# Kernel tuning notes

Hardware: AMD Instinct MI355X
Metric: run time of the kernel (lower is better)

Reference implementation:

```python
import jax, jax.numpy as jnp
import numpy as np

N_NODES = 40000
N_EDGES = 640000
IN_DIM, H_DIM, OUT_DIM = 128, 128, 64


def setup_inputs() -> dict:
    key = jax.random.key(0)
    ks = jax.random.split(key, 16)
    x = jax.random.normal(ks[0], (N_NODES, IN_DIM), dtype=jnp.float32)
    edge_index = jax.random.randint(ks[1], (2, N_EDGES), 0, N_NODES, dtype=jnp.int64)
    dims = [(IN_DIM, H_DIM), (H_DIM, H_DIM), (H_DIM, OUT_DIM)]
    inp = {"x": x, "edge_index": edge_index}
    for l, (di, do) in enumerate(dims):
        s = 1.0 / np.sqrt(di)
        inp[f"Wr{l}"] = jax.random.uniform(ks[2 + 3 * l], (di, do), jnp.float32, -s, s)  # lin_rel weight
        inp[f"br{l}"] = jax.random.uniform(ks[3 + 3 * l], (do,), jnp.float32, -s, s)     # lin_rel bias
        inp[f"Ws{l}"] = jax.random.uniform(ks[4 + 3 * l], (di, do), jnp.float32, -s, s)  # lin_root weight (no bias)
    return inp


def _graph_conv(x, src, dst, Wr, br, Ws):
    # PyG GraphConv (aggr='add'): out = lin_rel(sum_{j in N(i)} x_j) + lin_root(x_i)
    agg = jax.ops.segment_sum(x[src], dst, num_segments=N_NODES)  # [N, d_in]
    return agg @ Wr + br + x @ Ws


def reference(x, edge_index, Wr0, br0, Ws0, Wr1, br1, Ws1, Wr2, br2, Ws2):
    src, dst = edge_index[0], edge_index[1]
    h = x
    for Wr, br, Ws in ((Wr0, br0, Ws0), (Wr1, br1, Ws1), (Wr2, br2, Ws2)):
        h = _graph_conv(h, src, dst, Wr, br, Ws)
        h = jax.nn.relu(h)
        # dropout p=0 / eval mode -> identity
    return jax.nn.log_softmax(h, axis=1)
```

## Files before the change

kernel.cpp:

```cpp
#include <hip/hip_runtime.h>
#include <hip/hip_bf16.h>


#define N_NODES 40000
#define N_EDGES 640000
#define PAD_NODES 40064
#define DEG_CAP   40960
#define ROW_CAP   64

typedef float v4f __attribute__((ext_vector_type(4)));
typedef float v2f __attribute__((ext_vector_type(2)));
typedef short short8 __attribute__((ext_vector_type(8)));

__device__ inline unsigned short f2b(float f) {
    unsigned u = __float_as_uint(f);
    return (unsigned short)((u + 0x7fffu + ((u >> 16) & 1u)) >> 16);
}

__device__ inline unsigned b2f8(unsigned short us) {
    unsigned s  = ((unsigned)us >> 8) & 0x80u;
    unsigned mag = us & 0x7fffu;
    unsigned e8 = mag >> 7, m7 = mag & 0x7fu;
    unsigned out;
    if (e8 < 121u) out = 0u;
    else if (e8 > 135u) out = 0x7eu;
    else {
        unsigned e4 = e8 - 120u;
        unsigned r  = (m7 + 7u + ((m7 >> 4) & 1u)) >> 4;
        if (r == 8u) { r = 0u; e4++; }
        out = (e4 > 15u || (e4 == 15u && r > 6u)) ? 0x7eu : ((e4 << 3) | r);
    }
    return s | out;
}

__device__ inline unsigned pack4_fp8(float f0, float f1, float f2, float f3) {
#if __has_builtin(__builtin_amdgcn_cvt_pk_fp8_f32)
    int w = __builtin_amdgcn_cvt_pk_fp8_f32(f0, f1, 0, false);
    w = __builtin_amdgcn_cvt_pk_fp8_f32(f2, f3, w, true);
    return (unsigned)w;
#else
    return b2f8(f2b(f0)) | (b2f8(f2b(f1)) << 8) |
           (b2f8(f2b(f2)) << 16) | (b2f8(f2b(f3)) << 24);
#endif
}

#if __has_builtin(__builtin_amdgcn_cvt_f32_fp8)
#define F8TOF(w, sel) __builtin_amdgcn_cvt_f32_fp8((int)(w), (sel))
#else
__device__ inline float f8tof_(unsigned b) {
    unsigned e = (b >> 3) & 15u;
    unsigned bits = ((b & 0x80u) << 24) |
                    (e ? (((e + 120u) << 23) | ((b & 7u) << 20)) : 0u);
    return __uint_as_float(bits);
}
#define F8TOF(w, sel) f8tof_(((unsigned)(w) >> ((sel) * 8)) & 0xffu)
#endif

__global__ __launch_bounds__(256) void prep_kernel(const float* __restrict__ Wr0, const float* __restrict__ Ws0,
                                                   const float* __restrict__ Wr1, const float* __restrict__ Ws1,
                                                   const float* __restrict__ Wr2, const float* __restrict__ Ws2,
                                                   const float* __restrict__ x,
                                                   unsigned short* __restrict__ Wt0,
                                                   unsigned short* __restrict__ Wt1,
                                                   unsigned short* __restrict__ Wt2,
                                                   unsigned short* __restrict__ Xb,
                                                   int* __restrict__ deg) {
    int tid = blockIdx.x * 256 + threadIdx.x;
    if (tid < DEG_CAP / 4) {
        ((int4*)deg)[tid] = make_int4(0, 0, 0, 0);
        return;
    }
    int t = tid - DEG_CAP / 4;
    if (t < 32768) {
        int n = t >> 7, k = t & 127;
        const float* W = (n < 128) ? Wr0 : Ws0;
        Wt0[t] = f2b(W[k * 128 + (n & 127)]);
    } else if (t < 65536) {
        int u = t - 32768;
        int n = u >> 7, k = u & 127;
        const float* W = (n < 128) ? Wr1 : Ws1;
        Wt1[u] = f2b(W[k * 128 + (n & 127)]);
    } else if (t < 81920) {
        int u = t - 65536;
        int n = u >> 7, k = u & 127;
        const float* W = (n < 64) ? Wr2 : Ws2;
        Wt2[u] = f2b(W[k * 64 + (n & 63)]);
    } else {
        int u = t - 81920;
        if (u < (N_NODES * 128) / 8) {
            float4 a = ((const float4*)x)[u * 2];
            float4 b = ((const float4*)x)[u * 2 + 1];
            uint4 o;
            o.x = (unsigned)f2b(a.x) | ((unsigned)f2b(a.y) << 16);
            o.y = (unsigned)f2b(a.z) | ((unsigned)f2b(a.w) << 16);
            o.z = (unsigned)f2b(b.x) | ((unsigned)f2b(b.y) << 16);
            o.w = (unsigned)f2b(b.z) | ((unsigned)f2b(b.w) << 16);
            ((uint4*)Xb)[u] = o;
        }
    }
}

__global__ __launch_bounds__(256) void place_kernel(const int* __restrict__ src,
                                                    const int* __restrict__ dst,
                                                    int* __restrict__ deg,
                                                    int* __restrict__ esrc) {
    int e = blockIdx.x * 256 + threadIdx.x;
    if (e < N_EDGES) {
        int d = dst[e];
        int r = atomicAdd(&deg[d], 1);
        if (r < ROW_CAP) esrc[(size_t)d * ROW_CAP + r] = src[e];
    }
}

template <int DO>
__global__ __launch_bounds__(256, 6) void mm_kernel(const unsigned short* __restrict__ Ab,
                                                    const unsigned short* __restrict__ Wt,
                                                    void* __restrict__ Tout,
                                                    unsigned short* __restrict__ S) {
    __shared__ unsigned short Smem[64 * 64 + 128 * 64];
    unsigned short* As = Smem;
    unsigned short* Bs = Smem + 64 * 64;

    const int tid = threadIdx.x;
    const int m0  = blockIdx.x * 64;
    const int n0  = blockIdx.y * 128;

    const int wave = tid >> 6;
    const int lane = tid & 63;
    const int wc   = wave * 32;
    const int qm   = lane & 15;
    const int k8   = (lane >> 4) * 8;

    v4f acc[4][2];
#pragma unroll
    for (int i = 0; i < 4; i++)
#pragma unroll
        for (int j = 0; j < 2; j++) acc[i][j] = (v4f)(0.0f);

#pragma unroll
    for (int half = 0; half < 2; half++) {
#pragma unroll
        for (int i = 0; i < 2; i++) {
            int idx = i * 256 + tid;
            int row = idx >> 3, c8 = idx & 7;
            ((uint4*)As)[idx] =
                *(const uint4*)(Ab + (size_t)(m0 + row) * 128 + half * 64 + c8 * 8);
        }
#pragma unroll
        for (int i = 0; i < 4; i++) {
            int idx = i * 256 + tid;
            int row = idx >> 3, c8 = idx & 7;
            ((uint4*)Bs)[idx] =
                *(const uint4*)(Wt + (size_t)(n0 + row) * 128 + half * 64 + c8 * 8);
        }
        __syncthreads();

#pragma unroll
        for (int ks = 0; ks < 2; ks++) {
            short8 af[4], bf[2];
#pragma unroll
            for (int i = 0; i < 4; i++)
                af[i] = *(const short8*)(const void*)(As + (i * 16 + qm) * 64 + ks * 32 + k8);
#pragma unroll
            for (int j = 0; j < 2; j++)
                bf[j] = *(const short8*)(const void*)(Bs + (wc + j * 16 + qm) * 64 + ks * 32 + k8);
#pragma unroll
            for (int mi = 0; mi < 4; mi++)
#pragma unroll
                for (int ni = 0; ni < 2; ni++)
                    acc[mi][ni] = __builtin_amdgcn_mfma_f32_16x16x32_bf16(af[mi], bf[ni], acc[mi][ni], 0, 0, 0);
        }
        __syncthreads();
    }

#pragma unroll
    for (int mi = 0; mi < 4; mi++) {
        const int rowBase = mi * 16 + ((lane >> 4) << 2);
#pragma unroll
        for (int r = 0; r < 4; r++) {
            const int row = rowBase + r;
            const int sw  = ((row >> 2) & 3) << 4;
#pragma unroll
            for (int ni = 0; ni < 2; ni++) {
                const int c = wc + ni * 16 + qm;
                Smem[row * 128 + (c ^ sw)] = f2b(acc[mi][ni][r]);
            }
        }
    }
    __syncthreads();

    if (DO == 128 && n0 == 0) {
        unsigned char* T8 = (unsigned char*)Tout;
#pragma unroll
        for (int i = 0; i < 2; i++) {
            const int chunk = i * 256 + tid;
            const int row   = chunk >> 3;
            const int c0    = (chunk & 7) * 16;
            const int sw    = ((row >> 2) & 3) << 4;
            const int node  = m0 + row;
            if (node <= N_NODES) {
                uint4 v = make_uint4(0, 0, 0, 0);
                if (node < N_NODES) {
                    const unsigned short* p = Smem + row * 128 + (c0 ^ sw);
                    uint4 ha = *(const uint4*)p;
                    uint4 hb = *(const uint4*)(p + 8);
#define LOF(d) __uint_as_float((d) << 16)
#define HIF(d) __uint_as_float((d) & 0xffff0000u)
                    v.x = pack4_fp8(LOF(ha.x), HIF(ha.x), LOF(ha.y), HIF(ha.y));
                    v.y = pack4_fp8(LOF(ha.z), HIF(ha.z), LOF(ha.w), HIF(ha.w));
                    v.z = pack4_fp8(LOF(hb.x), HIF(hb.x), LOF(hb.y), HIF(hb.y));
                    v.w = pack4_fp8(LOF(hb.z), HIF(hb.z), LOF(hb.w), HIF(hb.w));
#undef LOF
#undef HIF
                }
                *(uint4*)(T8 + (size_t)node * 128 + c0) = v;
            }
        }
    } else {
        unsigned short* T = (unsigned short*)Tout;
#pragma unroll
        for (int i = 0; i < 4; i++) {
            const int chunk = i * 256 + tid;
            const int row   = chunk >> 4;
            const int c0    = (chunk & 15) * 8;
            const int sw    = ((row >> 2) & 3) << 4;
            const int node  = m0 + row;
            if (node <= N_NODES) {
                uint4 v = make_uint4(0, 0, 0, 0);
                if (node < N_NODES)
                    v = *(const uint4*)(Smem + row * 128 + (c0 ^ sw));
                if (DO == 128) {
                    *(uint4*)(S + (size_t)node * 128 + c0) = v;
                } else {
                    if (c0 < 64) *(uint4*)(T + (size_t)node * 64 + c0) = v;
                    else         *(uint4*)(S + (size_t)node * 64 + (c0 - 64)) = v;
                }
            }
        }
    }
}

__device__ inline void addp(v2f* a, uint4 q) {
    v2f t0 = { __uint_as_float(q.x << 16), __uint_as_float(q.x & 0xffff0000u) };
    v2f t1 = { __uint_as_float(q.y << 16), __uint_as_float(q.y & 0xffff0000u) };
    v2f t2 = { __uint_as_float(q.z << 16), __uint_as_float(q.z & 0xffff0000u) };
    v2f t3 = { __uint_as_float(q.w << 16), __uint_as_float(q.w & 0xffff0000u) };
    a[0] += t0; a[1] += t1; a[2] += t2; a[3] += t3;
}
__device__ inline void addp8w(v2f* a, unsigned w) {
    v2f t0 = { F8TOF(w, 0), F8TOF(w, 1) };
    v2f t1 = { F8TOF(w, 2), F8TOF(w, 3) };
    a[0] += t0; a[1] += t1;
}
__device__ inline void addp16(v2f* a, uint4 q) {
    addp8w(a + 0, q.x); addp8w(a + 2, q.y);
    addp8w(a + 4, q.z); addp8w(a + 6, q.w);
}

template <int DO, bool LAST, bool FP8T>
__global__ __launch_bounds__(256) void aggregate_kernel(const void* __restrict__ Tin,
                                                        const unsigned short* __restrict__ S,
                                                        const float* __restrict__ br,
                                                        const int* __restrict__ deg,
                                                        const int* __restrict__ esrc,
                                                        unsigned short* __restrict__ Hout,
                                                        float* __restrict__ Fout) {
    constexpr int DPL = FP8T ? 16 : 8;
    const int lane16 = threadIdx.x & 15;
    const int g      = lane16 >> 3;
    const int lane   = lane16 & 7;
    const int n      = blockIdx.x * 16 + (threadIdx.x >> 4);

    int cnt = deg[n];
    if (cnt > ROW_CAP) cnt = ROW_CAP;
    const int* erow = esrc + (size_t)n * ROW_CAP;
    const uint4* T4 = (const uint4*)Tin;

    v2f acc[DPL / 2];
#pragma unroll
    for (int i = 0; i < DPL / 2; i++) acc[i] = (v2f)(0.0f);

    for (int o = g * 8; o < cnt; o += 16) {
        int4 i0 = *(const int4*)(erow + o);
        int4 i1 = *(const int4*)(erow + o + 4);
        i0.x = (o + 0 < cnt) ? i0.x : N_NODES;
        i0.y = (o + 1 < cnt) ? i0.y : N_NODES;
        i0.z = (o + 2 < cnt) ? i0.z : N_NODES;
        i0.w = (o + 3 < cnt) ? i0.w : N_NODES;
        i1.x = (o + 4 < cnt) ? i1.x : N_NODES;
        i1.y = (o + 5 < cnt) ? i1.y : N_NODES;
        i1.z = (o + 6 < cnt) ? i1.z : N_NODES;
        i1.w = (o + 7 < cnt) ? i1.w : N_NODES;
        uint4 q0 = T4[(size_t)i0.x * 8 + lane];
        uint4 q1 = T4[(size_t)i0.y * 8 + lane];
        uint4 q2 = T4[(size_t)i0.z * 8 + lane];
        uint4 q3 = T4[(size_t)i0.w * 8 + lane];
        uint4 q4 = T4[(size_t)i1.x * 8 + lane];
        uint4 q5 = T4[(size_t)i1.y * 8 + lane];
        uint4 q6 = T4[(size_t)i1.z * 8 + lane];
        uint4 q7 = T4[(size_t)i1.w * 8 + lane];
        if (FP8T) {
            addp16(acc, q0); addp16(acc, q1); addp16(acc, q2); addp16(acc, q3);
            addp16(acc, q4); addp16(acc, q5); addp16(acc, q6); addp16(acc, q7);
        } else {
            addp(acc, q0); addp(acc, q1); addp(acc, q2); addp(acc, q3);
            addp(acc, q4); addp(acc, q5); addp(acc, q6); addp(acc, q7);
        }
    }

#pragma unroll
    for (int i = 0; i < DPL / 2; i++) {
        acc[i].x += __shfl_xor(acc[i].x, 8);
        acc[i].y += __shfl_xor(acc[i].y, 8);
    }

    float v[DPL];
#pragma unroll
    for (int h = 0; h < DPL / 8; h++) {
        uint4 sv = ((const uint4*)S)[(size_t)n * (DO / 8) + lane * (DPL / 8) + h];
        addp(acc + h * 4, sv);
    }
#pragma unroll
    for (int j = 0; j < DPL; j++) {
        float bj = br[lane * DPL + j];
        v[j] = fmaxf(((j & 1) ? acc[j >> 1].y : acc[j >> 1].x) + bj, 0.f);
    }

    if (LAST) {
        float m = v[0];
#pragma unroll
        for (int i = 1; i < 8; i++) m = fmaxf(m, v[i]);
#pragma unroll
        for (int off = 4; off; off >>= 1) m = fmaxf(m, __shfl_xor(m, off));
        float es = 0.f;
#pragma unroll
        for (int i = 0; i < 8; i++) es += expf(v[i] - m);
#pragma unroll
        for (int off = 4; off; off >>= 1) es += __shfl_xor(es, off);
        float lse = m + logf(es);
        if (g == 0) {
            float4 o0 = make_float4(v[0] - lse, v[1] - lse, v[2] - lse, v[3] - lse);
            float4 o1 = make_float4(v[4] - lse, v[5] - lse, v[6] - lse, v[7] - lse);
            ((float4*)Fout)[(size_t)n * 16 + lane * 2]     = o0;
            ((float4*)Fout)[(size_t)n * 16 + lane * 2 + 1] = o1;
        }
    } else if (g == 0) {
#pragma unroll
        for (int h = 0; h < DPL / 8; h++) {
            uint4 o;
            o.x = (unsigned)f2b(v[h * 8 + 0]) | ((unsigned)f2b(v[h * 8 + 1]) << 16);
            o.y = (unsigned)f2b(v[h * 8 + 2]) | ((unsigned)f2b(v[h * 8 + 3]) << 16);
            o.z = (unsigned)f2b(v[h * 8 + 4]) | ((unsigned)f2b(v[h * 8 + 5]) << 16);
            o.w = (unsigned)f2b(v[h * 8 + 6]) | ((unsigned)f2b(v[h * 8 + 7]) << 16);
            ((uint4*)Hout)[(size_t)n * (DO / 8) + lane * (DPL / 8) + h] = o;
        }
    }
}


extern "C" void kernel_launch(void* const* d_in, const int* in_sizes, int n_in,
                              void* d_out, int out_size, void* d_ws, size_t ws_size,
                              hipStream_t stream) {
    const float* x    = (const float*)d_in[0];
    const int*   eidx = (const int*)d_in[1];
    const float* Wr0  = (const float*)d_in[2];
    const float* br0  = (const float*)d_in[3];
    const float* Ws0  = (const float*)d_in[4];
    const float* Wr1  = (const float*)d_in[5];
    const float* br1  = (const float*)d_in[6];
    const float* Ws1  = (const float*)d_in[7];
    const float* Wr2  = (const float*)d_in[8];
    const float* br2  = (const float*)d_in[9];
    const float* Ws2  = (const float*)d_in[10];
    float* out = (float*)d_out;

    const int* src = eidx;
    const int* dst = eidx + N_EDGES;

    auto align = [](size_t v) { return (v + 255) & ~(size_t)255; };
    char* w = (char*)d_ws;
    int* deg  = (int*)w;  w += align(sizeof(int) * DEG_CAP);
    int* esrc = (int*)w;  w += align(sizeof(int) * (size_t)N_NODES * ROW_CAP);
    unsigned short* Xb  = (unsigned short*)w;  w += align(2ull * PAD_NODES * 128);
    unsigned short* H1b = (unsigned short*)w;  w += align(2ull * PAD_NODES * 128);
    unsigned short* H2b = (unsigned short*)w;  w += align(2ull * PAD_NODES * 128);
    unsigned short* Wt0 = (unsigned short*)w;  w += align(2ull * 256 * 128);
    unsigned short* Wt1 = (unsigned short*)w;  w += align(2ull * 256 * 128);
    unsigned short* Wt2 = (unsigned short*)w;  w += align(2ull * 128 * 128);
    void*           T   = (void*)w;            w += align(2ull * PAD_NODES * 128);
    unsigned short* Sb  = (unsigned short*)w;  w += align(2ull * PAD_NODES * 128);
    (void)ws_size; (void)n_in; (void)in_sizes; (void)out_size;

    prep_kernel<<<(DEG_CAP / 4 + 81920 + (N_NODES * 128) / 8 + 255) / 256, 256, 0, stream>>>(
        Wr0, Ws0, Wr1, Ws1, Wr2, Ws2, x, Wt0, Wt1, Wt2, Xb, deg);

    place_kernel<<<(N_EDGES + 255) / 256, 256, 0, stream>>>(src, dst, deg, esrc);

    mm_kernel<128><<<dim3(PAD_NODES / 64, 2), 256, 0, stream>>>(Xb, Wt0, T, Sb);
    aggregate_kernel<128, false, true><<<N_NODES / 16, 256, 0, stream>>>(T, Sb, br0, deg, esrc, H1b, nullptr);

    mm_kernel<128><<<dim3(PAD_NODES / 64, 2), 256, 0, stream>>>(H1b, Wt1, T, Sb);
    aggregate_kernel<128, false, true><<<N_NODES / 16, 256, 0, stream>>>(T, Sb, br1, deg, esrc, H2b, nullptr);

    mm_kernel<64><<<dim3(PAD_NODES / 64, 1), 256, 0, stream>>>(H2b, Wt2, T, Sb);
    aggregate_kernel<64, true, false><<<N_NODES / 16, 256, 0, stream>>>(T, Sb, br2, deg, esrc, nullptr, out);
}
```

Before: 199.5 us.

## Fuse neighbor aggregation of layer l into the matmul of layer l+1

The separate aggregate and matmul kernels for layers 0-1 and 1-2 are merged: each mmf block gathers its 64 nodes' neighbor rows from the fp8 T buffer, adds the root term, bias and ReLU, and writes the bf16 activations straight into shared memory as the GEMM A tile. The matmul now computes the full 256-wide (or 128-wide) output per block with swizzled LDS layouts instead of a 2-D grid. This drops two launches and the H1/H2 global round-trips. In exchange, gathering uses only 4 threads per node with a serial edge loop, occupancy drops (launch bounds 3), and the ping-pong T/S buffers are sized for the new layout.

```diff
diff --git a/kernel.cpp b/kernel.cpp
--- a/kernel.cpp
+++ b/kernel.cpp
@@ -55,6 +55,23 @@
 }
 #define F8TOF(w, sel) f8tof_(((unsigned)(w) >> ((sel) * 8)) & 0xffu)
 #endif
+
+__device__ inline void addp(v2f* a, uint4 q) {
+    v2f t0 = { __uint_as_float(q.x << 16), __uint_as_float(q.x & 0xffff0000u) };
+    v2f t1 = { __uint_as_float(q.y << 16), __uint_as_float(q.y & 0xffff0000u) };
+    v2f t2 = { __uint_as_float(q.z << 16), __uint_as_float(q.z & 0xffff0000u) };
+    v2f t3 = { __uint_as_float(q.w << 16), __uint_as_float(q.w & 0xffff0000u) };
+    a[0] += t0; a[1] += t1; a[2] += t2; a[3] += t3;
+}
+__device__ inline void addp8w(v2f* a, unsigned w) {
+    v2f t0 = { F8TOF(w, 0), F8TOF(w, 1) };
+    v2f t1 = { F8TOF(w, 2), F8TOF(w, 3) };
+    a[0] += t0; a[1] += t1;
+}
+__device__ inline void addp16(v2f* a, uint4 q) {
+    addp8w(a + 0, q.x); addp8w(a + 2, q.y);
+    addp8w(a + 4, q.z); addp8w(a + 6, q.w);
+}
 
 __global__ __launch_bounds__(256) void prep_kernel(const float* __restrict__ Wr0, const float* __restrict__ Ws0,
                                                    const float* __restrict__ Wr1, const float* __restrict__ Ws1,
@@ -112,85 +129,174 @@
     }
 }
 
-template <int DO>
-__global__ __launch_bounds__(256, 6) void mm_kernel(const unsigned short* __restrict__ Ab,
-                                                    const unsigned short* __restrict__ Wt,
-                                                    void* __restrict__ Tout,
-                                                    unsigned short* __restrict__ S) {
-    __shared__ unsigned short Smem[64 * 64 + 128 * 64];
-    unsigned short* As = Smem;
-    unsigned short* Bs = Smem + 64 * 64;
-
-    const int tid = threadIdx.x;
-    const int m0  = blockIdx.x * 64;
-    const int n0  = blockIdx.y * 128;
-
+template <int DO, bool AGG>
+__global__ __launch_bounds__(256, 3) void mmf_kernel(const void* __restrict__ Ain,
+                                                     const unsigned short* __restrict__ Sprev,
+                                                     const float* __restrict__ brp,
+                                                     const int* __restrict__ deg,
+                                                     const int* __restrict__ esrc,
+                                                     const unsigned short* __restrict__ Wt,
+                                                     void* __restrict__ Tout,
+                                                     unsigned short* __restrict__ Sout) {
+    constexpr int NB  = 2 * DO;
+    constexpr int NBW = NB / 4;
+    constexpr int CF  = NBW / 16;
+
+    __shared__ unsigned short AsMem[64 * 128];
+    __shared__ unsigned short BsMem[NB * 64];
+    uint4* As4 = (uint4*)AsMem;
+    uint4* Bs4 = (uint4*)BsMem;
+
+    const int tid  = threadIdx.x;
+    const int m0   = blockIdx.x * 64;
     const int wave = tid >> 6;
     const int lane = tid & 63;
-    const int wc   = wave * 32;
     const int qm   = lane & 15;
-    const int k8   = (lane >> 4) * 8;
-
-    v4f acc[4][2];
-#pragma unroll
-    for (int i = 0; i < 4; i++)
-#pragma unroll
-        for (int j = 0; j < 2; j++) acc[i][j] = (v4f)(0.0f);
-
-#pragma unroll
-    for (int half = 0; half < 2; half++) {
-#pragma unroll
-        for (int i = 0; i < 2; i++) {
-            int idx = i * 256 + tid;
-            int row = idx >> 3, c8 = idx & 7;
-            ((uint4*)As)[idx] =
-                *(const uint4*)(Ab + (size_t)(m0 + row) * 128 + half * 64 + c8 * 8);
-        }
+    const int hi   = lane >> 4;
+    const int wcb  = wave * NBW;
+
+#pragma unroll
+    for (int i = 0; i < NB * 8 / 256; i++) {
+        int idx = i * 256 + tid;
+        int row = idx >> 3, c8 = idx & 7;
+        Bs4[row * 8 + (c8 ^ (row & 7))] =
+            *(const uint4*)(Wt + (size_t)row * 128 + c8 * 8);
+    }
+
+    if (AGG) {
+        const int noderow = tid >> 2;
+        const int lane4   = tid & 3;
+        const int n       = m0 + noderow;
+        if (n < N_NODES) {
+            int cnt = deg[n];
+            if (cnt > ROW_CAP) cnt = ROW_CAP;
+            const int* erow = esrc + (size_t)n * ROW_CAP;
+            const uint4* T8 = (const uint4*)Ain;
+            v2f acc[16];
+#pragma unroll
+            for (int i = 0; i < 16; i++) acc[i] = (v2f)(0.0f);
+            for (int o = 0; o < cnt; o += 4) {
+                int4 i0 = *(const int4*)(erow + o);
+                i0.x = (o + 0 < cnt) ? i0.x : N_NODES;
+                i0.y = (o + 1 < cnt) ? i0.y : N_NODES;
+                i0.z = (o + 2 < cnt) ? i0.z : N_NODES;
+                i0.w = (o + 3 < cnt) ? i0.w : N_NODES;
+                size_t b0 = (size_t)i0.x * 8 + lane4 * 2;
+                size_t b1 = (size_t)i0.y * 8 + lane4 * 2;
+                size_t b2 = (size_t)i0.z * 8 + lane4 * 2;
+                size_t b3 = (size_t)i0.w * 8 + lane4 * 2;
+                uint4 qa0 = T8[b0], qb0 = T8[b0 + 1];
+                uint4 qa1 = T8[b1], qb1 = T8[b1 + 1];
+                uint4 qa2 = T8[b2], qb2 = T8[b2 + 1];
+                uint4 qa3 = T8[b3], qb3 = T8[b3 + 1];
+                addp16(acc, qa0); addp16(acc + 8, qb0);
+                addp16(acc, qa1); addp16(acc + 8, qb1);
+                addp16(acc, qa2); addp16(acc + 8, qb2);
+                addp16(acc, qa3); addp16(acc + 8, qb3);
+            }
+#pragma unroll
+            for (int h = 0; h < 4; h++) {
+                uint4 sv = ((const uint4*)Sprev)[(size_t)n * 16 + lane4 * 4 + h];
+                addp(acc + h * 4, sv);
+            }
+#pragma unroll
+            for (int h = 0; h < 4; h++) {
+                float vv[8];
+#pragma unroll
+                for (int j = 0; j < 8; j++) {
+                    int d = h * 8 + j;
+                    float bj = brp[lane4 * 32 + d];
+                    vv[j] = fmaxf(((d & 1) ? acc[d >> 1].y : acc[d >> 1].x) + bj, 0.f);
+                }
+                uint4 o;
+                o.x = (unsigned)f2b(vv[0]) | ((unsigned)f2b(vv[1]) << 16);
+                o.y = (unsigned)f2b(vv[2]) | ((unsigned)f2b(vv[3]) << 16);
+                o.z = (unsigned)f2b(vv[4]) | ((unsigned)f2b(vv[5]) << 16);
+                o.w = (unsigned)f2b(vv[6]) | ((unsigned)f2b(vv[7]) << 16);
+                As4[noderow * 16 + ((lane4 * 4 + h) ^ (noderow & 7))] = o;
+            }
+        } else {
+            uint4 z = make_uint4(0, 0, 0, 0);
+#pragma unroll
+            for (int h = 0; h < 4; h++)
+                As4[noderow * 16 + ((lane4 * 4 + h) ^ (noderow & 7))] = z;
+        }
+    } else {
+        const unsigned short* Ab = (const unsigned short*)Ain;
 #pragma unroll
         for (int i = 0; i < 4; i++) {
             int idx = i * 256 + tid;
-            int row = idx >> 3, c8 = idx & 7;
-            ((uint4*)Bs)[idx] =
-                *(const uint4*)(Wt + (size_t)(n0 + row) * 128 + half * 64 + c8 * 8);
-        }
-        __syncthreads();
-
+            int row = idx >> 4, c = idx & 15;
+            int gr = m0 + row;
+            if (gr > N_NODES - 1) gr = N_NODES - 1;
+            As4[row * 16 + (c ^ (row & 7))] =
+                *(const uint4*)(Ab + (size_t)gr * 128 + c * 8);
+        }
+    }
+    __syncthreads();
+
+    v4f acc[4][CF];
+#pragma unroll
+    for (int i = 0; i < 4; i++)
+#pragma unroll
+        for (int j = 0; j < CF; j++) acc[i][j] = (v4f)(0.0f);
+
+#pragma unroll
+    for (int half = 0; half < 2; half++) {
+        if (half == 1) {
+            __syncthreads();
+#pragma unroll
+            for (int i = 0; i < NB * 8 / 256; i++) {
+                int idx = i * 256 + tid;
+                int row = idx >> 3, c8 = idx & 7;
+                Bs4[row * 8 + (c8 ^ (row & 7))] =
+                    *(const uint4*)(Wt + (size_t)row * 128 + 64 + c8 * 8);
+            }
+            __syncthreads();
+        }
 #pragma unroll
         for (int ks = 0; ks < 2; ks++) {
-            short8 af[4], bf[2];
-#pragma unroll
-            for (int i = 0; i < 4; i++)
-                af[i] = *(const short8*)(const void*)(As + (i * 16 + qm) * 64 + ks * 32 + k8);
-#pragma unroll
-            for (int j = 0; j < 2; j++)
-                bf[j] = *(const short8*)(const void*)(Bs + (wc + j * 16 + qm) * 64 + ks * 32 + k8);
+            short8 af[4], bf[CF];
+#pragma unroll
+            for (int mi = 0; mi < 4; mi++) {
+                const int r  = mi * 16 + qm;
+                const int ca = half * 8 + ks * 4 + hi;
+                af[mi] = *(const short8*)&As4[r * 16 + (ca ^ (r & 7))];
+            }
+#pragma unroll
+            for (int ni = 0; ni < CF; ni++) {
+                const int rb = wcb + ni * 16 + qm;
+                const int cb = ks * 4 + hi;
+                bf[ni] = *(const short8*)&Bs4[rb * 8 + (cb ^ (rb & 7))];
+            }
 #pragma unroll
             for (int mi = 0; mi < 4; mi++)
 #pragma unroll
-                for (int ni = 0; ni < 2; ni++)
+                for (int ni = 0; ni < CF; ni++)
                     acc[mi][ni] = __builtin_amdgcn_mfma_f32_16x16x32_bf16(af[mi], bf[ni], acc[mi][ni], 0, 0, 0);
         }
-        __syncthreads();
-    }
-
+    }
+    __syncthreads();
+
+    unsigned short* Es = BsMem;
 #pragma unroll
     for (int mi = 0; mi < 4; mi++) {
-        const int rowBase = mi * 16 + ((lane >> 4) << 2);
+        const int rowBase = mi * 16 + (hi << 2);
 #pragma unroll
         for (int r = 0; r < 4; r++) {
             const int row = rowBase + r;
             const int sw  = ((row >> 2) & 3) << 4;
 #pragma unroll
-            for (int ni = 0; ni < 2; ni++) {
-                const int c = wc + ni * 16 + qm;
-                Smem[row * 128 + (c ^ sw)] = f2b(acc[mi][ni][r]);
+            for (int ni = 0; ni < CF; ni++) {
+                const int c = wcb + ni * 16 + qm;
+                Es[row * NB + (c ^ sw)] = f2b(acc[mi][ni][r]);
             }
         }
     }
     __syncthreads();
 
-    if (DO == 128 && n0 == 0) {
-        unsigned char* T8 = (unsigned char*)Tout;
+    if (DO == 128) {
+        unsigned char* T8o = (unsigned char*)Tout;
 #pragma unroll
         for (int i = 0; i < 2; i++) {
             const int chunk = i * 256 + tid;
@@ -201,7 +307,7 @@
             if (node <= N_NODES) {
                 uint4 v = make_uint4(0, 0, 0, 0);
                 if (node < N_NODES) {
-                    const unsigned short* p = Smem + row * 128 + (c0 ^ sw);
+                    const unsigned short* p = Es + row * 256 + (c0 ^ sw);
                     uint4 ha = *(const uint4*)p;
                     uint4 hb = *(const uint4*)(p + 8);
 #define LOF(d) __uint_as_float((d) << 16)
@@ -213,11 +319,25 @@
 #undef LOF
 #undef HIF
                 }
-                *(uint4*)(T8 + (size_t)node * 128 + c0) = v;
+                *(uint4*)(T8o + (size_t)node * 128 + c0) = v;
+            }
+        }
+#pragma unroll
+        for (int i = 0; i < 4; i++) {
+            const int chunk = i * 256 + tid;
+            const int row   = chunk >> 4;
+            const int c0    = 128 + (chunk & 15) * 8;
+            const int sw    = ((row >> 2) & 3) << 4;
+            const int node  = m0 + row;
+            if (node <= N_NODES) {
+                uint4 v = make_uint4(0, 0, 0, 0);
+                if (node < N_NODES)
+                    v = *(const uint4*)(Es + row * 256 + (c0 ^ sw));
+                *(uint4*)(Sout + (size_t)node * 128 + (c0 - 128)) = v;
             }
         }
     } else {
-        unsigned short* T = (unsigned short*)Tout;
+        unsigned short* Tb = (unsigned short*)Tout;
 #pragma unroll
         for (int i = 0; i < 4; i++) {
             const int chunk = i * 256 + tid;
@@ -228,44 +348,20 @@
             if (node <= N_NODES) {
                 uint4 v = make_uint4(0, 0, 0, 0);
                 if (node < N_NODES)
-                    v = *(const uint4*)(Smem + row * 128 + (c0 ^ sw));
-                if (DO == 128) {
-                    *(uint4*)(S + (size_t)node * 128 + c0) = v;
-                } else {
-                    if (c0 < 64) *(uint4*)(T + (size_t)node * 64 + c0) = v;
-                    else         *(uint4*)(S + (size_t)node * 64 + (c0 - 64)) = v;
-                }
-            }
-        }
-    }
-}
-
-__device__ inline void addp(v2f* a, uint4 q) {
-    v2f t0 = { __uint_as_float(q.x << 16), __uint_as_float(q.x & 0xffff0000u) };
-    v2f t1 = { __uint_as_float(q.y << 16), __uint_as_float(q.y & 0xffff0000u) };
-    v2f t2 = { __uint_as_float(q.z << 16), __uint_as_float(q.z & 0xffff0000u) };
-    v2f t3 = { __uint_as_float(q.w << 16), __uint_as_float(q.w & 0xffff0000u) };
-    a[0] += t0; a[1] += t1; a[2] += t2; a[3] += t3;
-}
-__device__ inline void addp8w(v2f* a, unsigned w) {
-    v2f t0 = { F8TOF(w, 0), F8TOF(w, 1) };
-    v2f t1 = { F8TOF(w, 2), F8TOF(w, 3) };
-    a[0] += t0; a[1] += t1;
-}
-__device__ inline void addp16(v2f* a, uint4 q) {
-    addp8w(a + 0, q.x); addp8w(a + 2, q.y);
-    addp8w(a + 4, q.z); addp8w(a + 6, q.w);
-}
-
-template <int DO, bool LAST, bool FP8T>
-__global__ __launch_bounds__(256) void aggregate_kernel(const void* __restrict__ Tin,
-                                                        const unsigned short* __restrict__ S,
-                                                        const float* __restrict__ br,
-                                                        const int* __restrict__ deg,
-                                                        const int* __restrict__ esrc,
-                                                        unsigned short* __restrict__ Hout,
-                                                        float* __restrict__ Fout) {
-    constexpr int DPL = FP8T ? 16 : 8;
+                    v = *(const uint4*)(Es + row * 128 + (c0 ^ sw));
+                if (c0 < 64) *(uint4*)(Tb + (size_t)node * 64 + c0) = v;
+                else         *(uint4*)(Sout + (size_t)node * 64 + (c0 - 64)) = v;
+            }
+        }
+    }
+}
+
+__global__ __launch_bounds__(256) void agg_last_kernel(const unsigned short* __restrict__ T,
+                                                       const unsigned short* __restrict__ S,
+                                                       const float* __restrict__ br,
+                                                       const int* __restrict__ deg,
+                                                       const int* __restrict__ esrc,
+                                                       float* __restrict__ Fout) {
     const int lane16 = threadIdx.x & 15;
     const int g      = lane16 >> 3;
     const int lane   = lane16 & 7;
@@ -274,11 +370,11 @@
     int cnt = deg[n];
     if (cnt > ROW_CAP) cnt = ROW_CAP;
     const int* erow = esrc + (size_t)n * ROW_CAP;
-    const uint4* T4 = (const uint4*)Tin;
-
-    v2f acc[DPL / 2];
-#pragma unroll
-    for (int i = 0; i < DPL / 2; i++) acc[i] = (v2f)(0.0f);
+    const uint4* T4 = (const uint4*)T;
+
+    v2f acc[4];
+    acc[0] = (v2f)(0.0f); acc[1] = (v2f)(0.0f);
+    acc[2] = (v2f)(0.0f); acc[3] = (v2f)(0.0f);
 
     for (int o = g * 8; o < cnt; o += 16) {
         int4 i0 = *(const int4*)(erow + o);
@@ -299,61 +395,42 @@
         uint4 q5 = T4[(size_t)i1.y * 8 + lane];
         uint4 q6 = T4[(size_t)i1.z * 8 + lane];
         uint4 q7 = T4[(size_t)i1.w * 8 + lane];
-        if (FP8T) {
-            addp16(acc, q0); addp16(acc, q1); addp16(acc, q2); addp16(acc, q3);
-            addp16(acc, q4); addp16(acc, q5); addp16(acc, q6); addp16(acc, q7);
-        } else {
-            addp(acc, q0); addp(acc, q1); addp(acc, q2); addp(acc, q3);
-            addp(acc, q4); addp(acc, q5); addp(acc, q6); addp(acc, q7);
-        }
-    }
-
-#pragma unroll
-    for (int i = 0; i < DPL / 2; i++) {
+        addp(acc, q0); addp(acc, q1); addp(acc, q2); addp(acc, q3);
+        addp(acc, q4); addp(acc, q5); addp(acc, q6); addp(acc, q7);
+    }
+#pragma unroll
+    for (int i = 0; i < 4; i++) {
         acc[i].x += __shfl_xor(acc[i].x, 8);
         acc[i].y += __shfl_xor(acc[i].y, 8);
     }
 
-    float v[DPL];
-#pragma unroll
-    for (int h = 0; h < DPL / 8; h++) {
-        uint4 sv = ((const uint4*)S)[(size_t)n * (DO / 8) + lane * (DPL / 8) + h];
-        addp(acc + h * 4, sv);
-    }
-#pragma unroll
-    for (int j = 0; j < DPL; j++) {
-        float bj = br[lane * DPL + j];
-        v[j] = fmaxf(((j & 1) ? acc[j >> 1].y : acc[j >> 1].x) + bj, 0.f);
-    }
-
-    if (LAST) {
-        float m = v[0];
-#pragma unroll
-        for (int i = 1; i < 8; i++) m = fmaxf(m, v[i]);
-#pragma unroll
-        for (int off = 4; off; off >>= 1) m = fmaxf(m, __shfl_xor(m, off));
-        float es = 0.f;
-#pragma unroll
-        for (int i = 0; i < 8; i++) es += expf(v[i] - m);
-#pragma unroll
-        for (int off = 4; off; off >>= 1) es += __shfl_xor(es, off);
-        float lse = m + logf(es);
-        if (g == 0) {
-            float4 o0 = make_float4(v[0] - lse, v[1] - lse, v[2] - lse, v[3] - lse);
-            float4 o1 = make_float4(v[4] - lse, v[5] - lse, v[6] - lse, v[7] - lse);
-            ((float4*)Fout)[(size_t)n * 16 + lane * 2]     = o0;
-            ((float4*)Fout)[(size_t)n * 16 + lane * 2 + 1] = o1;
-        }
-    } else if (g == 0) {
-#pragma unroll
-        for (int h = 0; h < DPL / 8; h++) {
-            uint4 o;
-            o.x = (unsigned)f2b(v[h * 8 + 0]) | ((unsigned)f2b(v[h * 8 + 1]) << 16);
-            o.y = (unsigned)f2b(v[h * 8 + 2]) | ((unsigned)f2b(v[h * 8 + 3]) << 16);
-            o.z = (unsigned)f2b(v[h * 8 + 4]) | ((unsigned)f2b(v[h * 8 + 5]) << 16);
-            o.w = (unsigned)f2b(v[h * 8 + 6]) | ((unsigned)f2b(v[h * 8 + 7]) << 16);
-            ((uint4*)Hout)[(size_t)n * (DO / 8) + lane * (DPL / 8) + h] = o;
-        }
+    uint4 sv = ((const uint4*)S)[(size_t)n * 8 + lane];
+    addp(acc, sv);
+    const float4 b0 = ((const float4*)br)[lane * 2];
+    const float4 b1 = ((const float4*)br)[lane * 2 + 1];
+
+    float v[8];
+    v[0] = fmaxf(acc[0].x + b0.x, 0.f); v[1] = fmaxf(acc[0].y + b0.y, 0.f);
+    v[2] = fmaxf(acc[1].x + b0.z, 0.f); v[3] = fmaxf(acc[1].y + b0.w, 0.f);
+    v[4] = fmaxf(acc[2].x + b1.x, 0.f); v[5] = fmaxf(acc[2].y + b1.y, 0.f);
+    v[6] = fmaxf(acc[3].x + b1.z, 0.f); v[7] = fmaxf(acc[3].y + b1.w, 0.f);
+
+    float m = v[0];
+#pragma unroll
+    for (int i = 1; i < 8; i++) m = fmaxf(m, v[i]);
+#pragma unroll
+    for (int off = 4; off; off >>= 1) m = fmaxf(m, __shfl_xor(m, off));
+    float es = 0.f;
+#pragma unroll
+    for (int i = 0; i < 8; i++) es += expf(v[i] - m);
+#pragma unroll
+    for (int off = 4; off; off >>= 1) es += __shfl_xor(es, off);
+    float lse = m + logf(es);
+    if (g == 0) {
+        float4 o0 = make_float4(v[0] - lse, v[1] - lse, v[2] - lse, v[3] - lse);
+        float4 o1 = make_float4(v[4] - lse, v[5] - lse, v[6] - lse, v[7] - lse);
+        ((float4*)Fout)[(size_t)n * 16 + lane * 2]     = o0;
+        ((float4*)Fout)[(size_t)n * 16 + lane * 2 + 1] = o1;
     }
 }
 
@@ -382,13 +459,13 @@
     int* deg  = (int*)w;  w += align(sizeof(int) * DEG_CAP);
     int* esrc = (int*)w;  w += align(sizeof(int) * (size_t)N_NODES * ROW_CAP);
     unsigned short* Xb  = (unsigned short*)w;  w += align(2ull * PAD_NODES * 128);
-    unsigned short* H1b = (unsigned short*)w;  w += align(2ull * PAD_NODES * 128);
-    unsigned short* H2b = (unsigned short*)w;  w += align(2ull * PAD_NODES * 128);
     unsigned short* Wt0 = (unsigned short*)w;  w += align(2ull * 256 * 128);
     unsigned short* Wt1 = (unsigned short*)w;  w += align(2ull * 256 * 128);
     unsigned short* Wt2 = (unsigned short*)w;  w += align(2ull * 128 * 128);
-    void*           T   = (void*)w;            w += align(2ull * PAD_NODES * 128);
-    unsigned short* Sb  = (unsigned short*)w;  w += align(2ull * PAD_NODES * 128);
+    void* T_a = (void*)w;                      w += align(2ull * PAD_NODES * 64);
+    void* T_b = (void*)w;                      w += align(2ull * PAD_NODES * 64);
+    unsigned short* S_a = (unsigned short*)w;  w += align(2ull * PAD_NODES * 128);
+    unsigned short* S_b = (unsigned short*)w;  w += align(2ull * PAD_NODES * 128);
     (void)ws_size; (void)n_in; (void)in_sizes; (void)out_size;
 
     prep_kernel<<<(DEG_CAP / 4 + 81920 + (N_NODES * 128) / 8 + 255) / 256, 256, 0, stream>>>(
@@ -396,12 +473,15 @@
 
     place_kernel<<<(N_EDGES + 255) / 256, 256, 0, stream>>>(src, dst, deg, esrc);
 
-    mm_kernel<128><<<dim3(PAD_NODES / 64, 2), 256, 0, stream>>>(Xb, Wt0, T, Sb);
-    aggregate_kernel<128, false, true><<<N_NODES / 16, 256, 0, stream>>>(T, Sb, br0, deg, esrc, H1b, nullptr);
-
-    mm_kernel<128><<<dim3(PAD_NODES / 64, 2), 256, 0, stream>>>(H1b, Wt1, T, Sb);
-    aggregate_kernel<128, false, true><<<N_NODES / 16, 256, 0, stream>>>(T, Sb, br1, deg, esrc, H2b, nullptr);
-
-    mm_kernel<64><<<dim3(PAD_NODES / 64, 1), 256, 0, stream>>>(H2b, Wt2, T, Sb);
-    aggregate_kernel<64, true, false><<<N_NODES / 16, 256, 0, stream>>>(T, Sb, br2, deg, esrc, nullptr, out);
-}
+    mmf_kernel<128, false><<<PAD_NODES / 64, 256, 0, stream>>>(
+        Xb, nullptr, nullptr, nullptr, nullptr, Wt0, T_a, S_a);
+
+    mmf_kernel<128, true><<<PAD_NODES / 64, 256, 0, stream>>>(
+        T_a, S_a, br0, deg, esrc, Wt1, T_b, S_b);
+
+    mmf_kernel<64, true><<<PAD_NODES / 64, 256, 0, stream>>>(
+        T_b, S_b, br1, deg, esrc, Wt2, T_a, S_a);
+
+    agg_last_kernel<<<N_NODES / 16, 256, 0, stream>>>(
+        (const unsigned short*)T_a, S_a, br2, deg, esrc, out);
+}
```

Measured after the change: 193.0 us. -3.2%, faster.
